# Performance work log

Hardware: AMD Instinct MI355X
Metric: run time of the kernel (lower is better)

Reference implementation:

```python
import jax, jax.numpy as jnp
import numpy as np

N_NODES = 100000
N_EDGES = 800000
F_IN = 128
H1, C1 = 8, 32
N_CLS = 40
NEG_SLOPE = 0.2


def setup_inputs() -> dict:
    key = jax.random.key(0)
    ks = jax.random.split(key, 10)
    s = 1.0 / np.sqrt(F_IN)
    s2 = 1.0 / np.sqrt(H1 * C1)
    return {
        "x": jax.random.normal(ks[0], (N_NODES, F_IN), jnp.float32),
        "edge_index": jax.random.randint(ks[1], (2, N_EDGES), 0, N_NODES, jnp.int64),
        "W1": jax.random.normal(ks[2], (F_IN, H1 * C1), jnp.float32) * s,
        "a_src1": jax.random.normal(ks[3], (H1, C1), jnp.float32) * s2,
        "a_dst1": jax.random.normal(ks[4], (H1, C1), jnp.float32) * s2,
        "b1": jnp.zeros((H1 * C1,), jnp.float32),
        "W2": jax.random.normal(ks[5], (H1 * C1, N_CLS), jnp.float32) * s2,
        "a_src2": jax.random.normal(ks[6], (1, N_CLS), jnp.float32) * 0.1,
        "a_dst2": jax.random.normal(ks[7], (1, N_CLS), jnp.float32) * 0.1,
        "b2": jnp.zeros((N_CLS,), jnp.float32),
    }


def gat_conv(x, src, dst, W, a_src, a_dst, b, heads, out_ch, concat):
    n = x.shape[0]
    h = (x @ W).reshape(n, heads, out_ch)            # [N,H,C]
    alpha_s = jnp.einsum("nhc,hc->nh", h, a_src)     # [N,H]
    alpha_d = jnp.einsum("nhc,hc->nh", h, a_dst)
    e = alpha_s[src] + alpha_d[dst]                  # [E,H]
    e = jax.nn.leaky_relu(e, NEG_SLOPE)
    # per-destination segment softmax (stable)
    m = jax.ops.segment_max(e, dst, num_segments=n)  # [N,H]
    e = jnp.exp(e - m[dst])
    denom = jax.ops.segment_sum(e, dst, num_segments=n)
    alpha = e / (denom[dst] + 1e-16)                 # [E,H]
    msg = alpha[:, :, None] * h[src]                 # [E,H,C]
    out = jax.ops.segment_sum(msg, dst, num_segments=n)  # [N,H,C]
    out = out.reshape(n, heads * out_ch) if concat else out.mean(axis=1)
    return out + b


def reference(x, edge_index, W1, a_src1, a_dst1, b1, W2, a_src2, a_dst2, b2):
    n = x.shape[0]
    # PyG GATConv default add_self_loops=True
    loop = jnp.arange(n, dtype=edge_index.dtype)
    src = jnp.concatenate([edge_index[0], loop])
    dst = jnp.concatenate([edge_index[1], loop])
    # dropout layers are identity in eval mode
    h = gat_conv(x, src, dst, W1, a_src1, a_dst1, b1, H1, C1, concat=True)
    h = jax.nn.elu(h)
    out = gat_conv(h, src, dst, W2, a_src2, a_dst2, b2, 1, N_CLS, concat=False)
    return jax.nn.log_softmax(out, axis=1)
```

## Files before the change

### kernel.cpp

```cpp
#include <hip/hip_runtime.h>
#include <hip/hip_fp16.h>
#include <math.h>

#define N_NODESc 100000
#define N_EDGESc 800000
#define F_INc    128
#define HC1c     256
#define NCLSc    40
#define NEG_SLOPEc 0.2f
#define CAPc     40

typedef _Float16 half8 __attribute__((ext_vector_type(8)));
typedef __fp16   f16x2 __attribute__((ext_vector_type(2)));
typedef float    f32x4 __attribute__((ext_vector_type(4)));
typedef float    f32x2 __attribute__((ext_vector_type(2)));

__device__ __forceinline__ unsigned pack_ws(float w, int src) {
    union { f16x2 h; unsigned u; } t;
    t.h = __builtin_amdgcn_cvt_pkrtz(w, w);
    return (unsigned)src | ((t.u & 0xFFFFu) << 17);
}
__device__ __forceinline__ float unpack_w(unsigned pe) {
    union { unsigned short s; __fp16 h; } t;
    t.s = (unsigned short)(pe >> 17);
    return (float)t.h;
}


__global__ void k_init(const float* __restrict__ W1, const float* __restrict__ W2,
                       _Float16* __restrict__ W1Tf, _Float16* __restrict__ W2Tf,
                       int* __restrict__ cnt, int* __restrict__ bucket) {
    if (blockIdx.x < 22) {
        int f = blockIdx.x * 256 + threadIdx.x;
        if (f < 4096) {
            int lane16 = f & 15, quad = (f >> 4) & 3, k0 = (f >> 6) & 3, jt = f >> 8;
            int c = lane16 * 16 + jt;
            int kbase = k0 * 32 + quad * 8;
            _Float16* o = W1Tf + (size_t)f * 8;
            #pragma unroll
            for (int j = 0; j < 8; j++) o[j] = (_Float16)W1[(kbase + j) * HC1c + c];
        } else if (f < 4096 + 1536) {
            int g = f - 4096;
            int lane16 = g & 15, quad = (g >> 4) & 3, k0 = (g >> 6) & 7, jt = g >> 9;
            int c = jt * 16 + lane16;
            int kbase = k0 * 32 + quad * 8;
            _Float16* o = W2Tf + (size_t)g * 8;
            #pragma unroll
            for (int j = 0; j < 8; j++)
                o[j] = (c < NCLSc) ? (_Float16)W2[(kbase + j) * NCLSc + c] : (_Float16)0.f;
        }
    } else {
        int i = (blockIdx.x - 22) * 256 + threadIdx.x;
        if (i < N_NODESc) {
            cnt[i] = 1;
            bucket[i * CAPc] = i;
        }
    }
}


__global__ void k_scatter(const int* __restrict__ src, const int* __restrict__ dst,
                          int* __restrict__ cnt, int* __restrict__ bucket) {
    int i = blockIdx.x * blockDim.x + threadIdx.x;
    if (i < N_EDGESc / 2) {
        int2 s = ((const int2*)src)[i];
        int2 d = ((const int2*)dst)[i];
        int p0 = atomicAdd(&cnt[d.x], 1);
        if (p0 < CAPc) bucket[d.x * CAPc + p0] = s.x;
        int p1 = atomicAdd(&cnt[d.y], 1);
        if (p1 < CAPc) bucket[d.y * CAPc + p1] = s.y;
    }
}


__global__ __launch_bounds__(256) void k_gemm1(
    const float* __restrict__ x, const _Float16* __restrict__ W1Tf,
    const float* __restrict__ a_src1, const float* __restrict__ a_dst1,
    unsigned char* __restrict__ h1f8, float* __restrict__ as1, float* __restrict__ ad1) {
    int wave = (blockIdx.x * 256 + threadIdx.x) >> 6;
    int n0 = wave * 16;
    if (n0 >= N_NODESc) return;
    int L = threadIdx.x & 63, lane16 = L & 15, quad = L >> 4;
    f32x4 acc[16];
    #pragma unroll
    for (int jt = 0; jt < 16; jt++) acc[jt] = (f32x4){0.f, 0.f, 0.f, 0.f};
    const float* A = x + (size_t)(n0 + lane16) * F_INc + quad * 8;
    const _Float16* Bf = W1Tf + L * 8;
    #pragma unroll
    for (int k0 = 0; k0 < 4; k0++) {
        float4 f0 = *(const float4*)(A + k0 * 32);
        float4 f1 = *(const float4*)(A + k0 * 32 + 4);
        union { half8 v; f16x2 h[4]; } af;
        af.h[0] = __builtin_amdgcn_cvt_pkrtz(f0.x, f0.y);
        af.h[1] = __builtin_amdgcn_cvt_pkrtz(f0.z, f0.w);
        af.h[2] = __builtin_amdgcn_cvt_pkrtz(f1.x, f1.y);
        af.h[3] = __builtin_amdgcn_cvt_pkrtz(f1.z, f1.w);
        #pragma unroll
        for (int jt = 0; jt < 16; jt++) {
            half8 bf = *(const half8*)(Bf + (jt * 4 + k0) * 512);
            acc[jt] = __builtin_amdgcn_mfma_f32_16x16x32_f16(af.v, bf, acc[jt], 0, 0, 0);
        }
    }
    {
        #pragma unroll
        for (int r = 0; r < 4; r++) {
            uint4 st;
            int d;
            d = __builtin_amdgcn_cvt_pk_fp8_f32(acc[0][r], acc[1][r], 0, false);
            d = __builtin_amdgcn_cvt_pk_fp8_f32(acc[2][r], acc[3][r], d, true);
            st.x = (unsigned)d;
            d = __builtin_amdgcn_cvt_pk_fp8_f32(acc[4][r], acc[5][r], 0, false);
            d = __builtin_amdgcn_cvt_pk_fp8_f32(acc[6][r], acc[7][r], d, true);
            st.y = (unsigned)d;
            d = __builtin_amdgcn_cvt_pk_fp8_f32(acc[8][r], acc[9][r], 0, false);
            d = __builtin_amdgcn_cvt_pk_fp8_f32(acc[10][r], acc[11][r], d, true);
            st.z = (unsigned)d;
            d = __builtin_amdgcn_cvt_pk_fp8_f32(acc[12][r], acc[13][r], 0, false);
            d = __builtin_amdgcn_cvt_pk_fp8_f32(acc[14][r], acc[15][r], d, true);
            st.w = (unsigned)d;
            *(uint4*)(h1f8 + (size_t)(n0 + quad * 4 + r) * HC1c + lane16 * 16) = st;
        }
    }
    {
        float asv[16], adv[16];
        const float4* ap = (const float4*)(a_src1 + lane16 * 16);
        const float4* dp = (const float4*)(a_dst1 + lane16 * 16);
        #pragma unroll
        for (int q = 0; q < 4; q++) {
            float4 a4 = ap[q], d4 = dp[q];
            asv[4*q] = a4.x; asv[4*q+1] = a4.y; asv[4*q+2] = a4.z; asv[4*q+3] = a4.w;
            adv[4*q] = d4.x; adv[4*q+1] = d4.y; adv[4*q+2] = d4.z; adv[4*q+3] = d4.w;
        }
        float ps[4] = {0,0,0,0}, pd[4] = {0,0,0,0};
        #pragma unroll
        for (int jt = 0; jt < 16; jt++) {
            #pragma unroll
            for (int r = 0; r < 4; r++) {
                ps[r] += acc[jt][r] * asv[jt];
                pd[r] += acc[jt][r] * adv[jt];
            }
        }
        #pragma unroll
        for (int r = 0; r < 4; r++) {
            ps[r] += __shfl_xor(ps[r], 1);
            pd[r] += __shfl_xor(pd[r], 1);
        }
        if ((lane16 & 1) == 0) {
            int h = lane16 >> 1;
            #pragma unroll
            for (int r = 0; r < 4; r++) {
                int n = n0 + quad * 4 + r;
                as1[n * 8 + h] = ps[r];
                ad1[n * 8 + h] = pd[r];
            }
        }
    }
}


__global__ __launch_bounds__(256) void k_agg1(
    const int* __restrict__ cnt, const int* __restrict__ bucket,
    const float* __restrict__ as1, const float* __restrict__ ad1,
    const unsigned char* __restrict__ h1f8, const float* __restrict__ b1,
    _Float16* __restrict__ act1b) {
    int n = blockIdx.x * 4 + (threadIdx.x >> 6);
    if (n >= N_NODESc) return;
    int L = threadIdx.x & 63;
    int eL = L >> 3, hL = L & 7;
    int hA = L >> 3;
    int beg = n * CAPc;
    int end = beg + min(cnt[n], CAPc);
    float ad = ad1[n * 8 + hL];
    float m_run = -INFINITY, d_run = 0.f;
    f32x2 accA = (f32x2){0.f, 0.f};
    f32x2 accB = (f32x2){0.f, 0.f};
    for (int base = beg; base < end; base += 16) {
        int m = min(16, end - base);
        int src0 = 0, src1 = 0;
        float s0 = -INFINITY, s1 = -INFINITY;
        if (eL < m) {
            src0 = bucket[base + eL];
            float v = as1[src0 * 8 + hL] + ad;
            s0 = (v > 0.f) ? v : NEG_SLOPEc * v;
        }
        if (eL + 8 < m) {
            src1 = bucket[base + eL + 8];
            float v = as1[src1 * 8 + hL] + ad;
            s1 = (v > 0.f) ? v : NEG_SLOPEc * v;
        }
        float mc = fmaxf(s0, s1);
        mc = fmaxf(mc, __shfl_xor(mc, 8));
        mc = fmaxf(mc, __shfl_xor(mc, 16));
        mc = fmaxf(mc, __shfl_xor(mc, 32));
        float mnew = fmaxf(m_run, mc);
        float w0 = (eL < m) ? __expf(s0 - mnew) : 0.f;
        float w1 = (eL + 8 < m) ? __expf(s1 - mnew) : 0.f;
        float wsum = w0 + w1;
        wsum += __shfl_xor(wsum, 8);
        wsum += __shfl_xor(wsum, 16);
        wsum += __shfl_xor(wsum, 32);
        float scale = __expf(m_run - mnew);
        d_run = d_run * scale + wsum;
        m_run = mnew;
        float sc = __shfl(scale, hA);
        f32x2 sc2 = (f32x2){sc, sc};
        accA *= sc2;
        accB *= sc2;
        unsigned pk0 = pack_ws(w0, src0);
        unsigned pk1 = pack_ws(w1, src1);
        #pragma unroll
        for (int r = 0; r < 4; r++) {
            int e0 = r * 4;
            if (e0 < m) {
                unsigned pk = (e0 < 8) ? pk0 : pk1;
                unsigned pe[4]; unsigned ld[4];
                #pragma unroll
                for (int j = 0; j < 4; j++)
                    pe[j] = __shfl(pk, ((e0 + j) & 7) * 8 + hA);
                #pragma unroll
                for (int j = 0; j < 4; j++)
                    ld[j] = *((const unsigned*)(h1f8 + (size_t)(pe[j] & 0x1FFFFu) * HC1c) + L);
                #pragma unroll
                for (int j = 0; j < 4; j++) {
                    float w = unpack_w(pe[j]);
                    f32x2 wv = (f32x2){w, w};
                    f32x2 lo = __builtin_amdgcn_cvt_pk_f32_fp8((int)ld[j], false);
                    f32x2 hi = __builtin_amdgcn_cvt_pk_f32_fp8((int)ld[j], true);
                    asm("v_pk_fma_f32 %0, %1, %2, %0" : "+v"(accA) : "v"(wv), "v"(lo));
                    asm("v_pk_fma_f32 %0, %1, %2, %0" : "+v"(accB) : "v"(wv), "v"(hi));
                }
            }
        }
    }
    float inv = __builtin_amdgcn_rcpf(d_run + 1e-16f);
    float inv_h = __shfl(inv, hA);
    float4 bb = ((const float4*)b1)[L];
    float o0 = accA[0] * inv_h + bb.x;
    float o1 = accA[1] * inv_h + bb.y;
    float o2 = accB[0] * inv_h + bb.z;
    float o3 = accB[1] * inv_h + bb.w;
    o0 = (o0 > 0.f) ? o0 : (__expf(o0) - 1.f);
    o1 = (o1 > 0.f) ? o1 : (__expf(o1) - 1.f);
    o2 = (o2 > 0.f) ? o2 : (__expf(o2) - 1.f);
    o3 = (o3 > 0.f) ? o3 : (__expf(o3) - 1.f);
    union { uint2 u; f16x2 h[2]; } st;
    st.h[0] = __builtin_amdgcn_cvt_pkrtz(o0, o1);
    st.h[1] = __builtin_amdgcn_cvt_pkrtz(o2, o3);
    ((uint2*)(act1b + (size_t)n * HC1c))[L] = st.u;
}


__global__ __launch_bounds__(256) void k_gemm2(
    const _Float16* __restrict__ act1b, const _Float16* __restrict__ W2Tf,
    const float* __restrict__ a_src2, const float* __restrict__ a_dst2,
    _Float16* __restrict__ h2b, float* __restrict__ as2, float* __restrict__ ad2) {
    int wave = (blockIdx.x * 256 + threadIdx.x) >> 6;
    int n0 = wave * 16;
    if (n0 >= N_NODESc) return;
    int L = threadIdx.x & 63, lane16 = L & 15, quad = L >> 4;
    f32x4 acc[3];
    #pragma unroll
    for (int jt = 0; jt < 3; jt++) acc[jt] = (f32x4){0.f, 0.f, 0.f, 0.f};
    const _Float16* A = act1b + (size_t)(n0 + lane16) * HC1c + quad * 8;
    const _Float16* Bf = W2Tf + L * 8;
    #pragma unroll
    for (int k0 = 0; k0 < 8; k0++) {
        half8 af = *(const half8*)(A + k0 * 32);
        #pragma unroll
        for (int jt = 0; jt < 3; jt++) {
            half8 bf = *(const half8*)(Bf + (jt * 8 + k0) * 512);
            acc[jt] = __builtin_amdgcn_mfma_f32_16x16x32_f16(af, bf, acc[jt], 0, 0, 0);
        }
    }
    float ps[4] = {0.f, 0.f, 0.f, 0.f}, pd[4] = {0.f, 0.f, 0.f, 0.f};
    #pragma unroll
    for (int jt = 0; jt < 3; jt++) {
        int col = jt * 16 + lane16;
        float ws = (col < NCLSc) ? a_src2[col] : 0.f;
        float wd = (col < NCLSc) ? a_dst2[col] : 0.f;
        #pragma unroll
        for (int r = 0; r < 4; r++) {
            float v = acc[jt][r];
            int n = n0 + quad * 4 + r;
            if (col < NCLSc) h2b[(size_t)n * NCLSc + col] = (_Float16)v;
            ps[r] += v * ws; pd[r] += v * wd;
        }
    }
    #pragma unroll
    for (int r = 0; r < 4; r++) {
        float s = ps[r], d = pd[r];
        s += __shfl_xor(s, 1); d += __shfl_xor(d, 1);
        s += __shfl_xor(s, 2); d += __shfl_xor(d, 2);
        s += __shfl_xor(s, 4); d += __shfl_xor(d, 4);
        s += __shfl_xor(s, 8); d += __shfl_xor(d, 8);
        if (lane16 == 0) {
            int n = n0 + quad * 4 + r;
            as2[n] = s; ad2[n] = d;
        }
    }
}


__global__ __launch_bounds__(256) void k_agg2(
    const int* __restrict__ cnt, const int* __restrict__ bucket,
    const float* __restrict__ as2, const float* __restrict__ ad2,
    const _Float16* __restrict__ h2b, const float* __restrict__ b2,
    float* __restrict__ out) {
    int n = blockIdx.x * 4 + (threadIdx.x >> 6);
    if (n >= N_NODESc) return;
    int L = threadIdx.x & 63;
    int g = L / 20, cls = L % 20;
    int beg = n * CAPc;
    int end = beg + min(cnt[n], CAPc);
    float ad = ad2[n];
    float m_run = -INFINITY, d_run = 0.f;
    f16x2 acc2 = (f16x2){(__fp16)0.f, (__fp16)0.f};
    for (int base = beg; base < end; base += 64) {
        int m = min(64, end - base);
        int src = 0; float s = -INFINITY;
        if (L < m) {
            src = bucket[base + L];
            float v = as2[src] + ad;
            s = (v > 0.f) ? v : NEG_SLOPEc * v;
        }
        float mc = s;
        for (int o = 32; o; o >>= 1) mc = fmaxf(mc, __shfl_xor(mc, o));
        float mnew = fmaxf(m_run, mc);
        float w = (L < m) ? __expf(s - mnew) : 0.f;
        float ws = w;
        for (int o = 32; o; o >>= 1) ws += __shfl_xor(ws, o);
        float scale = __expf(m_run - mnew);
        d_run = d_run * scale + ws;
        m_run = mnew;
        f16x2 sc2 = __builtin_amdgcn_cvt_pkrtz(scale, scale);
        acc2 *= sc2;
        for (int jb = 0; jb < m; jb += 9) {
            float wv[3]; int sev[3]; unsigned ldv[3];
            #pragma unroll
            for (int r = 0; r < 3; r++) {
                int e = jb + r * 3 + g;
                int lane = (e < 64) ? e : 63;
                wv[r] = __shfl(w, lane);
                sev[r] = __shfl(src, lane);
            }
            #pragma unroll
            for (int r = 0; r < 3; r++) {
                ldv[r] = 0u;
                if (g < 3)
                    ldv[r] = *((const unsigned*)(h2b + (size_t)sev[r] * NCLSc) + cls);
            }
            #pragma unroll
            for (int r = 0; r < 3; r++) {
                f16x2 we2 = __builtin_amdgcn_cvt_pkrtz(wv[r], wv[r]);
                union { unsigned u; f16x2 h; } pk; pk.u = ldv[r];
                acc2 += we2 * pk.h;
            }
        }
    }
    union { f16x2 h; int i; } au; au.h = acc2;
    int i1 = __shfl(au.i, (L + 20) & 63);
    int i2 = __shfl(au.i, (L + 40) & 63);
    union { int i; f16x2 h; } b1u, b2u; b1u.i = i1; b2u.i = i2;
    acc2 = acc2 + b1u.h + b2u.h;
    float vx = -INFINITY, vy = -INFINITY;
    if (L < 20) {
        float2 bb = ((const float2*)b2)[L];
        float inv = __builtin_amdgcn_rcpf(d_run + 1e-16f);
        vx = (float)acc2[0] * inv + bb.x;
        vy = (float)acc2[1] * inv + bb.y;
    }
    float mv = fmaxf(vx, vy);
    for (int o = 32; o; o >>= 1) mv = fmaxf(mv, __shfl_xor(mv, o));
    float ex = (L < 20) ? __expf(vx - mv) + __expf(vy - mv) : 0.f;
    for (int o = 32; o; o >>= 1) ex += __shfl_xor(ex, o);
    float ls = __logf(ex);
    if (L < 20) {
        float2 o2; o2.x = vx - mv - ls; o2.y = vy - mv - ls;
        ((float2*)(out + (size_t)n * NCLSc))[L] = o2;
    }
}


extern "C" void kernel_launch(void* const* d_in, const int* in_sizes, int n_in,
                              void* d_out, int out_size, void* d_ws, size_t ws_size,
                              hipStream_t stream) {
    const float* x    = (const float*)d_in[0];
    const int*   ei   = (const int*)d_in[1];
    const float* W1   = (const float*)d_in[2];
    const float* as1w = (const float*)d_in[3];
    const float* ad1w = (const float*)d_in[4];
    const float* b1   = (const float*)d_in[5];
    const float* W2   = (const float*)d_in[6];
    const float* as2w = (const float*)d_in[7];
    const float* ad2w = (const float*)d_in[8];
    const float* b2   = (const float*)d_in[9];
    float* out = (float*)d_out;

    char* p = (char*)d_ws;
    unsigned char* h1f8 = (unsigned char*)p; p += (size_t)N_NODESc * HC1c;
    _Float16* act1b = (_Float16*)p; p += (size_t)N_NODESc * HC1c * 2;
    _Float16* W1Tf  = (_Float16*)p; p += (size_t)4096 * 8 * 2;
    _Float16* W2Tf  = (_Float16*)p; p += (size_t)1536 * 8 * 2;
    float* a_s1 = (float*)p; p += (size_t)N_NODESc * 8 * 4;
    float* a_d1 = (float*)p; p += (size_t)N_NODESc * 8 * 4;
    _Float16* h2b = (_Float16*)p; p += (size_t)N_NODESc * NCLSc * 2;
    float* a_s2 = (float*)p; p += (size_t)N_NODESc * 4;
    float* a_d2 = (float*)p; p += (size_t)N_NODESc * 4;
    int* cnt    = (int*)p;   p += (size_t)N_NODESc * 4;
    int* bucket = (int*)p;   p += (size_t)N_NODESc * CAPc * 4;
    (void)ws_size; (void)in_sizes; (void)n_in; (void)out_size;

    const int* src = ei;
    const int* dst = ei + N_EDGESc;

    k_init<<<22 + (N_NODESc + 255) / 256, 256, 0, stream>>>(
        W1, W2, W1Tf, W2Tf, cnt, bucket);
    k_scatter<<<(N_EDGESc / 2 + 255) / 256, 256, 0, stream>>>(src, dst, cnt, bucket);

    int nwave_blk = ((N_NODESc + 15) / 16 + 3) / 4;
    k_gemm1<<<nwave_blk, 256, 0, stream>>>(x, W1Tf, as1w, ad1w, h1f8, a_s1, a_d1);
    k_agg1<<<(N_NODESc + 3) / 4, 256, 0, stream>>>(cnt, bucket, a_s1, a_d1, h1f8, b1, act1b);
    k_gemm2<<<nwave_blk, 256, 0, stream>>>(act1b, W2Tf, as2w, ad2w, h2b, a_s2, a_d2);
    k_agg2<<<(N_NODESc + 3) / 4, 256, 0, stream>>>(cnt, bucket, a_s2, a_d2, h2b, b2, out);
}
```

Before: 306.1 us.

## Fuse edge scatter into GEMM1 launch and handle self-loops in-register

The edge-bucketing scatter now runs inside the first GEMM kernel: even blocks do the atomic scatter and odd blocks do the GEMM, so the atomics overlap with matrix work and one launch is removed. Self-loops are no longer stored in the buckets. Each aggregation kernel seeds its online softmax with the node's own score and feature row instead, which drops a bucket write per node and one gathered edge per node. As a side effect, each bucket now holds up to CAP real neighbours, so behaviour changes slightly when a node overflows the capacity.

```diff
diff --git a/kernel.cpp b/kernel.cpp
--- a/kernel.cpp
+++ b/kernel.cpp
@@ -29,7 +29,7 @@
 
 __global__ void k_init(const float* __restrict__ W1, const float* __restrict__ W2,
                        _Float16* __restrict__ W1Tf, _Float16* __restrict__ W2Tf,
-                       int* __restrict__ cnt, int* __restrict__ bucket) {
+                       int* __restrict__ cnt) {
     if (blockIdx.x < 22) {
         int f = blockIdx.x * 256 + threadIdx.x;
         if (f < 4096) {
@@ -51,33 +51,30 @@
         }
     } else {
         int i = (blockIdx.x - 22) * 256 + threadIdx.x;
-        if (i < N_NODESc) {
-            cnt[i] = 1;
-            bucket[i * CAPc] = i;
-        }
-    }
-}
-
-
-__global__ void k_scatter(const int* __restrict__ src, const int* __restrict__ dst,
-                          int* __restrict__ cnt, int* __restrict__ bucket) {
-    int i = blockIdx.x * blockDim.x + threadIdx.x;
-    if (i < N_EDGESc / 2) {
-        int2 s = ((const int2*)src)[i];
-        int2 d = ((const int2*)dst)[i];
-        int p0 = atomicAdd(&cnt[d.x], 1);
-        if (p0 < CAPc) bucket[d.x * CAPc + p0] = s.x;
-        int p1 = atomicAdd(&cnt[d.y], 1);
-        if (p1 < CAPc) bucket[d.y * CAPc + p1] = s.y;
-    }
-}
-
-
-__global__ __launch_bounds__(256) void k_gemm1(
+        if (i < N_NODESc) cnt[i] = 0;
+    }
+}
+
+
+__global__ __launch_bounds__(256) void k_gemm1_scatter(
     const float* __restrict__ x, const _Float16* __restrict__ W1Tf,
     const float* __restrict__ a_src1, const float* __restrict__ a_dst1,
-    unsigned char* __restrict__ h1f8, float* __restrict__ as1, float* __restrict__ ad1) {
-    int wave = (blockIdx.x * 256 + threadIdx.x) >> 6;
+    unsigned char* __restrict__ h1f8, float* __restrict__ as1, float* __restrict__ ad1,
+    const int* __restrict__ src, const int* __restrict__ dst,
+    int* __restrict__ cnt, int* __restrict__ bucket) {
+    if ((blockIdx.x & 1) == 0) {
+        int i = (blockIdx.x >> 1) * 256 + threadIdx.x;
+        if (i < N_EDGESc / 2) {
+            int2 s = ((const int2*)src)[i];
+            int2 d = ((const int2*)dst)[i];
+            int p0 = atomicAdd(&cnt[d.x], 1);
+            if (p0 < CAPc) bucket[d.x * CAPc + p0] = s.x;
+            int p1 = atomicAdd(&cnt[d.y], 1);
+            if (p1 < CAPc) bucket[d.y * CAPc + p1] = s.y;
+        }
+        return;
+    }
+    int wave = ((blockIdx.x >> 1) * 256 + threadIdx.x) >> 6;
     int n0 = wave * 16;
     if (n0 >= N_NODESc) return;
     int L = threadIdx.x & 63, lane16 = L & 15, quad = L >> 4;
@@ -171,9 +168,12 @@
     int beg = n * CAPc;
     int end = beg + min(cnt[n], CAPc);
     float ad = ad1[n * 8 + hL];
-    float m_run = -INFINITY, d_run = 0.f;
-    f32x2 accA = (f32x2){0.f, 0.f};
-    f32x2 accB = (f32x2){0.f, 0.f};
+    float vs = as1[n * 8 + hL] + ad;
+    float s_self = (vs > 0.f) ? vs : NEG_SLOPEc * vs;
+    float m_run = s_self, d_run = 1.f;
+    unsigned ldself = *((const unsigned*)(h1f8 + (size_t)n * HC1c) + L);
+    f32x2 accA = __builtin_amdgcn_cvt_pk_f32_fp8((int)ldself, false);
+    f32x2 accB = __builtin_amdgcn_cvt_pk_f32_fp8((int)ldself, true);
     for (int base = beg; base < end; base += 16) {
         int m = min(16, end - base);
         int src0 = 0, src1 = 0;
@@ -313,8 +313,15 @@
     int beg = n * CAPc;
     int end = beg + min(cnt[n], CAPc);
     float ad = ad2[n];
-    float m_run = -INFINITY, d_run = 0.f;
+    float vs = as2[n] + ad;
+    float s_self = (vs > 0.f) ? vs : NEG_SLOPEc * vs;
+    float m_run = s_self, d_run = 1.f;
     f16x2 acc2 = (f16x2){(__fp16)0.f, (__fp16)0.f};
+    if (g == 0) {
+        union { unsigned u; f16x2 h; } pk;
+        pk.u = *((const unsigned*)(h2b + (size_t)n * NCLSc) + cls);
+        acc2 = pk.h;
+    }
     for (int base = beg; base < end; base += 64) {
         int m = min(64, end - base);
         int src = 0; float s = -INFINITY;
@@ -413,12 +420,13 @@
     const int* src = ei;
     const int* dst = ei + N_EDGESc;
 
-    k_init<<<22 + (N_NODESc + 255) / 256, 256, 0, stream>>>(
-        W1, W2, W1Tf, W2Tf, cnt, bucket);
-    k_scatter<<<(N_EDGESc / 2 + 255) / 256, 256, 0, stream>>>(src, dst, cnt, bucket);
-
+    k_init<<<22 + (N_NODESc + 255) / 256, 256, 0, stream>>>(W1, W2, W1Tf, W2Tf, cnt);
+
+    int nb_scat = (N_EDGESc / 2 + 255) / 256;
     int nwave_blk = ((N_NODESc + 15) / 16 + 3) / 4;
-    k_gemm1<<<nwave_blk, 256, 0, stream>>>(x, W1Tf, as1w, ad1w, h1f8, a_s1, a_d1);
+    k_gemm1_scatter<<<nb_scat + nwave_blk, 256, 0, stream>>>(
+        x, W1Tf, as1w, ad1w, h1f8, a_s1, a_d1, src, dst, cnt, bucket);
+
     k_agg1<<<(N_NODESc + 3) / 4, 256, 0, stream>>>(cnt, bucket, a_s1, a_d1, h1f8, b1, act1b);
     k_gemm2<<<nwave_blk, 256, 0, stream>>>(act1b, W2Tf, as2w, ad2w, h2b, a_s2, a_d2);
     k_agg2<<<(N_NODESc + 3) / 4, 256, 0, stream>>>(cnt, bucket, a_s2, a_d2, h2b, b2, out);
```

New measurement: 296.9 us. 3.0% less time.
